# Kernel tuning notes

Hardware: AMD Instinct MI355X
Metric: run time of the kernel (lower is better)

Reference implementation:

```python
import jax, jax.numpy as jnp
import numpy as np

CELL = 16          # pixels_per_cell
ORI = 6            # orientations
BIN_W = 180.0 / ORI
EPS = 1e-5         # skimage block-norm eps


def setup_inputs() -> dict:
    key = jax.random.key(0)
    x = jax.random.normal(key, (32, 3, 512, 512), dtype=jnp.float32)
    return {"x": x}


def _hog(x):
    # x: (B, 3, H, W) -> per-image HOG feature vector, matching skimage.feature.hog
    img = jnp.transpose(x, (0, 2, 3, 1))
    gray = 0.299 * img[..., 0] + 0.587 * img[..., 1] + 0.114 * img[..., 2]  # (B,H,W)
    B, H, W = gray.shape

    # skimage central-difference gradients with zeroed borders
    g_row = jnp.zeros_like(gray).at[:, 1:-1, :].set(gray[:, 2:, :] - gray[:, :-2, :])
    g_col = jnp.zeros_like(gray).at[:, :, 1:-1].set(gray[:, :, 2:] - gray[:, :, :-2])

    mag = jnp.hypot(g_row, g_col)
    ori = jnp.degrees(jnp.arctan2(g_row, g_col)) % 180.0
    bins = jnp.clip(jnp.floor(ori / BIN_W).astype(jnp.int32), 0, ORI - 1)

    # hard-assigned orientation histogram per 16x16 cell, averaged over cell pixels
    weighted = jax.nn.one_hot(bins, ORI, dtype=mag.dtype) * mag[..., None]  # (B,H,W,ORI)
    ncr, ncc = H // CELL, W // CELL
    cells = weighted.reshape(B, ncr, CELL, ncc, CELL, ORI).sum(axis=(2, 4)) / (CELL * CELL)

    # 2x2-cell blocks with stride 1 cell: (B, nbr, nbc, 2, 2, ORI)
    blocks = jnp.stack(
        [jnp.stack([cells[:, :-1, :-1], cells[:, :-1, 1:]], axis=3),
         jnp.stack([cells[:, 1:, :-1], cells[:, 1:, 1:]], axis=3)],
        axis=3)

    # L2-Hys normalization
    n1 = jnp.sqrt(jnp.sum(blocks * blocks, axis=(3, 4, 5), keepdims=True) + EPS * EPS)
    nb = jnp.minimum(blocks / n1, 0.2)
    n2 = jnp.sqrt(jnp.sum(nb * nb, axis=(3, 4, 5), keepdims=True) + EPS * EPS)
    nb = nb / n2
    return nb.reshape(B, -1).astype(jnp.float32)


def reference(x):
    return _hog(x)
```

## Files before the change

### kernel.cpp

```cpp
#include <hip/hip_runtime.h>
#include <math.h>

#define BATCH 32
#define HH 512
#define WW 512
#define NC 32
#define NORI 6
#define CH 262144

__device__ __forceinline__ int bin_of(float a) {
    const float deg = __fmul_rn(a, 57.29577951308232f);
    float m = fmodf(deg, 180.0f);
    if (m < 0.0f) m = __fadd_rn(m, 180.0f);
    const int b = (int)floorf(__fdiv_rn(m, 30.0f));
    return min(max(b, 0), NORI - 1);
}
__device__ __forceinline__ float ulp_step(float x, int k) {
    const int i = __float_as_int(x);
    int key = (i >= 0) ? i : -(i & 0x7FFFFFFF);
    key += k;
    const int r = (key >= 0) ? key : (int)(0x80000000u | (unsigned)(-key));
    return __int_as_float(r);
}
__device__ __forceinline__ void deposit(float acc[NORI], int bin, float val) {
#pragma unroll
    for (int o = 0; o < NORI; ++o) acc[o] += (bin == o) ? val : 0.0f;
}
__device__ __forceinline__ float gray_comb(float r, float g, float b) {
    return __fadd_rn(__fadd_rn(__fmul_rn(0.299f, r), __fmul_rn(0.587f, g)),
                     __fmul_rn(0.114f, b));
}
__device__ __forceinline__ float gray_i(const float* __restrict__ img, int off) {
    return gray_comb(img[off], img[off + CH], img[off + 2 * CH]);
}
__device__ __forceinline__ float4 gray4(const float* __restrict__ img, int off) {
    const float4 r = *(const float4*)(img + off);
    const float4 g = *(const float4*)(img + off + CH);
    const float4 b = *(const float4*)(img + off + 2 * CH);
    float4 o;
    o.x = gray_comb(r.x, g.x, b.x);
    o.y = gray_comb(r.y, g.y, b.y);
    o.z = gray_comb(r.z, g.z, b.z);
    o.w = gray_comb(r.w, g.w, b.w);
    return o;
}

__device__ __forceinline__ void hot_pixel(float gy, float gx, int bitk,
                                          float acc[NORI], unsigned& ambmask) {
    const float mag = __fsqrt_rn(__fmaf_rn(gy, gy, __fmul_rn(gx, gx)));
    const bool neg = gy < 0.0f;
    const float cy = fabsf(gy);
    const float cx = neg ? -gx : gx;
    const float pa = __fmul_rn(cy, 0.86602540378443864676f);
    const float pb = __fmul_rn(cx, 0.5f);
    const float pc = __fmul_rn(cy, 0.5f);
    const float pd = __fmul_rn(cx, 0.86602540378443864676f);
    const float t1 = __fsub_rn(pa, pb);
    const float t2 = __fsub_rn(pc, pd);
    const float t3 = -cx;
    const float t4 = -__fadd_rn(pc, pd);
    const float t5 = -__fadd_rn(pa, pb);
    int bin = (t1 >= 0.0f) + (t2 >= 0.0f) + (t3 >= 0.0f) +
              (t4 >= 0.0f) + (t5 >= 0.0f);
    const float s = __fmul_rn(mag, 1e-5f);
    const float mn = fminf(fminf(fminf(fabsf(t1), fabsf(t2)),
                                 fminf(fabsf(t3), fabsf(t4))), fabsf(t5));
    bool amb = (mn < s) || (cx < 0.0f && cy < s);
    if (gy == 0.0f) { bin = 0; amb = false; }
    else if (gx == 0.0f) { bin = 3; amb = false; }
    ambmask |= amb ? (1u << bitk) : 0u;
    deposit(acc, bin, amb ? 0.0f : mag);
}

__global__ __launch_bounds__(256) void hog_cells_kernel(const float* __restrict__ x,
                                                        float* __restrict__ cells) {
    const int b = blockIdx.z;
    const int tid = threadIdx.x;
    const int wave = tid >> 6, lane = tid & 63;
    const int by = blockIdx.y;
    const int R0 = by * 16 + wave * 4;
    const int C0 = blockIdx.x * 256;
    const int c0 = C0 + lane * 4;
    const float* img = x + (size_t)b * 3 * HH * WW;

    __shared__ float hist[16][NORI];
    if (tid < 16 * NORI) ((float*)hist)[tid] = 0.0f;
    __syncthreads();

    const bool left_blk = (blockIdx.x == 0);
    const int hc = left_blk ? 256 : 255;
    const bool is_h = (lane == (left_blk ? 63 : 0));

    float4 gm1 = gray4(img, max(R0 - 1, 0) * WW + c0);
    float4 g0  = gray4(img, R0 * WW + c0);
    float hcur = is_h ? gray_i(img, R0 * WW + hc) : 0.0f;

    float acc[NORI] = {0, 0, 0, 0, 0, 0};
    unsigned ambmask = 0;

#pragma unroll
    for (int k = 0; k < 4; ++k) {
        const int r = R0 + k;
        const int rn = min(r + 1, HH - 1);
        const float4 gp1 = gray4(img, rn * WW + c0);
        const float hnext = is_h ? gray_i(img, rn * WW + hc) : 0.0f;

        const bool row_ok = (r >= 1) && (r < HH - 1);
        const float gy0 = row_ok ? __fsub_rn(gp1.x, gm1.x) : 0.0f;
        const float gy1 = row_ok ? __fsub_rn(gp1.y, gm1.y) : 0.0f;
        const float gy2 = row_ok ? __fsub_rn(gp1.z, gm1.z) : 0.0f;
        const float gy3 = row_ok ? __fsub_rn(gp1.w, gm1.w) : 0.0f;

        float left  = __shfl(g0.w, (lane + 63) & 63);
        float right = __shfl(g0.x, (lane + 1) & 63);
        if (is_h) { if (left_blk) right = hcur; else left = hcur; }

        float gx0 = __fsub_rn(g0.y, left);
        const float gx1 = __fsub_rn(g0.z, g0.x);
        const float gx2 = __fsub_rn(g0.w, g0.y);
        float gx3 = __fsub_rn(right, g0.z);
        if (c0 == 0) gx0 = 0.0f;
        if (c0 + 3 == WW - 1) gx3 = 0.0f;

        hot_pixel(gy0, gx0, 4 * k + 0, acc, ambmask);
        hot_pixel(gy1, gx1, 4 * k + 1, acc, ambmask);
        hot_pixel(gy2, gx2, 4 * k + 2, acc, ambmask);
        hot_pixel(gy3, gx3, 4 * k + 3, acc, ambmask);

        gm1 = g0; g0 = gp1; hcur = hnext;
    }

    if (__any(ambmask != 0)) {
        unsigned m = ambmask;
        while (m) {
            const int bit = __builtin_ctz(m);
            m &= m - 1;
            const int r = R0 + (bit >> 2);
            const int c = c0 + (bit & 3);
            const int off = r * WW + c;
            const float gy = __fsub_rn(gray_i(img, off + WW), gray_i(img, off - WW));
            const float gx = __fsub_rn(gray_i(img, off + 1), gray_i(img, off - 1));
            const float mag = __fsqrt_rn(__fmaf_rn(gy, gy, __fmul_rn(gx, gx)));
            const float a = atan2f(gy, gx);
            const int bl = bin_of(ulp_step(a, -2));
            const int bh = bin_of(ulp_step(a, +2));
            if (bl == bh) {
                deposit(acc, bl, mag);
            } else {
                const int b0 = bin_of(a);
                const int bo = (b0 == bl) ? bh : bl;
                deposit(acc, b0, __fmul_rn(mag, 0.65f));
                deposit(acc, bo, __fmul_rn(mag, 0.35f));
            }
        }
    }

#pragma unroll
    for (int o = 0; o < NORI; ++o) {
        float v = acc[o];
        v += __shfl_xor(v, 1);
        v += __shfl_xor(v, 2);
        acc[o] = v;
    }
    if ((lane & 3) == 0) {
        const int cell = lane >> 2;
#pragma unroll
        for (int o = 0; o < NORI; ++o) atomicAdd(&hist[cell][o], acc[o]);
    }
    __syncthreads();
    if (tid < 96) {
        const int cell = tid / 6, o = tid - cell * 6;
        cells[(((size_t)b * NC + by) * NC + ((C0 >> 4) + cell)) * NORI + o] =
            hist[cell][o] * (1.0f / 256.0f);
    }
}

__global__ __launch_bounds__(256) void hog_norm_kernel(const float* __restrict__ cells,
                                                       float* __restrict__ out) {
    const int idx = blockIdx.x * 256 + threadIdx.x;
    const int total = BATCH * 31 * 31;
    if (idx >= total) return;
    const int bc = idx % 31;
    const int t = idx / 31;
    const int br = t % 31;
    const int b = t / 31;

    const float* cb = cells + (size_t)b * NC * NC * NORI;
    const float2* p0 = (const float2*)(cb + ((br) * NC + bc) * NORI);
    const float2* p1 = (const float2*)(cb + ((br + 1) * NC + bc) * NORI);
    float v[24];
#pragma unroll
    for (int q = 0; q < 6; ++q) {
        const float2 r0 = p0[q], r1 = p1[q];
        v[2 * q] = r0.x; v[2 * q + 1] = r0.y;
        v[12 + 2 * q] = r1.x; v[12 + 2 * q + 1] = r1.y;
    }
    float ss = 0.0f;
#pragma unroll
    for (int k = 0; k < 24; ++k) ss = __fadd_rn(ss, __fmul_rn(v[k], v[k]));
    const float n1 = __fsqrt_rn(__fadd_rn(ss, 1e-10f));
    float ss2 = 0.0f;
#pragma unroll
    for (int k = 0; k < 24; ++k) {
        v[k] = fminf(__fdiv_rn(v[k], n1), 0.2f);
        ss2 = __fadd_rn(ss2, __fmul_rn(v[k], v[k]));
    }
    const float n2 = __fsqrt_rn(__fadd_rn(ss2, 1e-10f));
    float* op = out + (size_t)idx * 24;
#pragma unroll
    for (int k = 0; k < 24; ++k) op[k] = __fdiv_rn(v[k], n2);
}

extern "C" void kernel_launch(void* const* d_in, const int* in_sizes, int n_in,
                              void* d_out, int out_size, void* d_ws, size_t ws_size,
                              hipStream_t stream) {
    const float* x = (const float*)d_in[0];
    float* out = (float*)d_out;
    float* cells = (float*)d_ws;

    dim3 g1(2, NC, BATCH), b1(256);
    hog_cells_kernel<<<g1, b1, 0, stream>>>(x, cells);

    const int total = BATCH * 31 * 31;
    hog_norm_kernel<<<(total + 255) / 256, 256, 0, stream>>>(cells, out);
}
```

Before: 151.7 us.

## Process full image width per block with eight pixels per thread

```diff
diff --git a/kernel.cpp b/kernel.cpp
--- a/kernel.cpp
+++ b/kernel.cpp
@@ -74,26 +74,23 @@
 
 __global__ __launch_bounds__(256) void hog_cells_kernel(const float* __restrict__ x,
                                                         float* __restrict__ cells) {
-    const int b = blockIdx.z;
+    const int b = blockIdx.y;
+    const int cr = blockIdx.x;
     const int tid = threadIdx.x;
     const int wave = tid >> 6, lane = tid & 63;
-    const int by = blockIdx.y;
-    const int R0 = by * 16 + wave * 4;
-    const int C0 = blockIdx.x * 256;
-    const int c0 = C0 + lane * 4;
+    const int R0 = cr * 16 + wave * 4;
+    const int c0 = lane * 8;
     const float* img = x + (size_t)b * 3 * HH * WW;
 
-    __shared__ float hist[16][NORI];
-    if (tid < 16 * NORI) ((float*)hist)[tid] = 0.0f;
+    __shared__ float hist[NC][NORI];
+    if (tid < NC * NORI) ((float*)hist)[tid] = 0.0f;
     __syncthreads();
 
-    const bool left_blk = (blockIdx.x == 0);
-    const int hc = left_blk ? 256 : 255;
-    const bool is_h = (lane == (left_blk ? 63 : 0));
-
-    float4 gm1 = gray4(img, max(R0 - 1, 0) * WW + c0);
-    float4 g0  = gray4(img, R0 * WW + c0);
-    float hcur = is_h ? gray_i(img, R0 * WW + hc) : 0.0f;
+    const int rm = max(R0 - 1, 0);
+    float4 gm1a = gray4(img, rm * WW + c0);
+    float4 gm1b = gray4(img, rm * WW + c0 + 4);
+    float4 g0a  = gray4(img, R0 * WW + c0);
+    float4 g0b  = gray4(img, R0 * WW + c0 + 4);
 
     float acc[NORI] = {0, 0, 0, 0, 0, 0};
     unsigned ambmask = 0;
@@ -102,32 +99,41 @@
     for (int k = 0; k < 4; ++k) {
         const int r = R0 + k;
         const int rn = min(r + 1, HH - 1);
-        const float4 gp1 = gray4(img, rn * WW + c0);
-        const float hnext = is_h ? gray_i(img, rn * WW + hc) : 0.0f;
+        const float4 gp1a = gray4(img, rn * WW + c0);
+        const float4 gp1b = gray4(img, rn * WW + c0 + 4);
 
         const bool row_ok = (r >= 1) && (r < HH - 1);
-        const float gy0 = row_ok ? __fsub_rn(gp1.x, gm1.x) : 0.0f;
-        const float gy1 = row_ok ? __fsub_rn(gp1.y, gm1.y) : 0.0f;
-        const float gy2 = row_ok ? __fsub_rn(gp1.z, gm1.z) : 0.0f;
-        const float gy3 = row_ok ? __fsub_rn(gp1.w, gm1.w) : 0.0f;
-
-        float left  = __shfl(g0.w, (lane + 63) & 63);
-        float right = __shfl(g0.x, (lane + 1) & 63);
-        if (is_h) { if (left_blk) right = hcur; else left = hcur; }
-
-        float gx0 = __fsub_rn(g0.y, left);
-        const float gx1 = __fsub_rn(g0.z, g0.x);
-        const float gx2 = __fsub_rn(g0.w, g0.y);
-        float gx3 = __fsub_rn(right, g0.z);
-        if (c0 == 0) gx0 = 0.0f;
-        if (c0 + 3 == WW - 1) gx3 = 0.0f;
-
-        hot_pixel(gy0, gx0, 4 * k + 0, acc, ambmask);
-        hot_pixel(gy1, gx1, 4 * k + 1, acc, ambmask);
-        hot_pixel(gy2, gx2, 4 * k + 2, acc, ambmask);
-        hot_pixel(gy3, gx3, 4 * k + 3, acc, ambmask);
-
-        gm1 = g0; g0 = gp1; hcur = hnext;
+        const float gy0 = row_ok ? __fsub_rn(gp1a.x, gm1a.x) : 0.0f;
+        const float gy1 = row_ok ? __fsub_rn(gp1a.y, gm1a.y) : 0.0f;
+        const float gy2 = row_ok ? __fsub_rn(gp1a.z, gm1a.z) : 0.0f;
+        const float gy3 = row_ok ? __fsub_rn(gp1a.w, gm1a.w) : 0.0f;
+        const float gy4 = row_ok ? __fsub_rn(gp1b.x, gm1b.x) : 0.0f;
+        const float gy5 = row_ok ? __fsub_rn(gp1b.y, gm1b.y) : 0.0f;
+        const float gy6 = row_ok ? __fsub_rn(gp1b.z, gm1b.z) : 0.0f;
+        const float gy7 = row_ok ? __fsub_rn(gp1b.w, gm1b.w) : 0.0f;
+
+        const float left  = __shfl(g0b.w, (lane + 63) & 63);
+        const float right = __shfl(g0a.x, (lane + 1) & 63);
+
+        const float gx0 = (lane == 0)  ? 0.0f : __fsub_rn(g0a.y, left);
+        const float gx1 = __fsub_rn(g0a.z, g0a.x);
+        const float gx2 = __fsub_rn(g0a.w, g0a.y);
+        const float gx3 = __fsub_rn(g0b.x, g0a.z);
+        const float gx4 = __fsub_rn(g0b.y, g0a.w);
+        const float gx5 = __fsub_rn(g0b.z, g0b.x);
+        const float gx6 = __fsub_rn(g0b.w, g0b.y);
+        const float gx7 = (lane == 63) ? 0.0f : __fsub_rn(right, g0b.z);
+
+        hot_pixel(gy0, gx0, 8 * k + 0, acc, ambmask);
+        hot_pixel(gy1, gx1, 8 * k + 1, acc, ambmask);
+        hot_pixel(gy2, gx2, 8 * k + 2, acc, ambmask);
+        hot_pixel(gy3, gx3, 8 * k + 3, acc, ambmask);
+        hot_pixel(gy4, gx4, 8 * k + 4, acc, ambmask);
+        hot_pixel(gy5, gx5, 8 * k + 5, acc, ambmask);
+        hot_pixel(gy6, gx6, 8 * k + 6, acc, ambmask);
+        hot_pixel(gy7, gx7, 8 * k + 7, acc, ambmask);
+
+        gm1a = g0a; gm1b = g0b; g0a = gp1a; g0b = gp1b;
     }
 
     if (__any(ambmask != 0)) {
@@ -135,8 +141,8 @@
         while (m) {
             const int bit = __builtin_ctz(m);
             m &= m - 1;
-            const int r = R0 + (bit >> 2);
-            const int c = c0 + (bit & 3);
+            const int r = R0 + (bit >> 3);
+            const int c = c0 + (bit & 7);
             const int off = r * WW + c;
             const float gy = __fsub_rn(gray_i(img, off + WW), gray_i(img, off - WW));
             const float gx = __fsub_rn(gray_i(img, off + 1), gray_i(img, off - 1));
@@ -159,18 +165,17 @@
     for (int o = 0; o < NORI; ++o) {
         float v = acc[o];
         v += __shfl_xor(v, 1);
-        v += __shfl_xor(v, 2);
         acc[o] = v;
     }
-    if ((lane & 3) == 0) {
-        const int cell = lane >> 2;
+    if ((lane & 1) == 0) {
+        const int cell = lane >> 1;
 #pragma unroll
         for (int o = 0; o < NORI; ++o) atomicAdd(&hist[cell][o], acc[o]);
     }
     __syncthreads();
-    if (tid < 96) {
+    if (tid < NC * NORI) {
         const int cell = tid / 6, o = tid - cell * 6;
-        cells[(((size_t)b * NC + by) * NC + ((C0 >> 4) + cell)) * NORI + o] =
+        cells[(((size_t)b * NC + cr) * NC + cell) * NORI + o] =
             hist[cell][o] * (1.0f / 256.0f);
     }
 }
@@ -218,7 +223,7 @@
     float* out = (float*)d_out;
     float* cells = (float*)d_ws;
 
-    dim3 g1(2, NC, BATCH), b1(256);
+    dim3 g1(NC, BATCH), b1(256);
     hog_cells_kernel<<<g1, b1, 0, stream>>>(x, cells);
 
     const int total = BATCH * 31 * 31;
```

New measurement: 156.8 us. +3.3%, slower.
